# Performance work log

Hardware: AMD Instinct MI355X
Metric: run time of the kernel (lower is better)

Reference implementation:

```python
import jax, jax.numpy as jnp
import numpy as np

B, L, D, W = 4, 256, 256, 8  # batch, seq_len, d_model, context_window
NS_EPS = 1e-7


def setup_inputs() -> dict:
    key = jax.random.key(0)
    ks = jax.random.split(key, 12)
    f = lambda k, s: jax.random.normal(k, s, dtype=jnp.float32)
    sD = 1.0 / np.sqrt(D)
    return {
        "x": f(ks[0], (B, L, D)),
        "k_aligned": jnp.tanh(f(ks[1], (B, L, D))),  # QKProjectionLayer applies tanh upstream
        "v": f(ks[2], (B, L, D)),
        "M_prev": f(ks[3], (B, D, D)) * 0.01,
        "S_prev": jnp.zeros((B, D, D), jnp.float32),
        # polynomial feature coeffs: phi(k) = c1*k + c2*k^2 (degree 2, dim-preserving)
        "poly_coeffs": jnp.stack([jnp.ones((D,), jnp.float32), 0.1 * jnp.ones((D,), jnp.float32)])
        + 0.01 * f(ks[4], (2, D)),
        "alpha_W": f(ks[5], (D, D)) * sD, "alpha_b": jnp.zeros((D,), jnp.float32),
        "eta_W": f(ks[6], (D, D)) * sD, "eta_b": jnp.zeros((D,), jnp.float32),
        "theta_W": f(ks[7], (D, D)) * sD, "theta_b": jnp.zeros((D,), jnp.float32),
        "gamma_W": f(ks[8], (D,)) * sD, "gamma_b": jnp.zeros((1,), jnp.float32),
        "out_W": f(ks[9], (D, D)) * sD, "out_b": jnp.zeros((D,), jnp.float32),
    }


def _newton_schulz_1(S):
    # NS_K with K=1: X <- 1.5*X - 0.5*X X^T X after Frobenius normalization
    norm = jnp.sqrt(jnp.sum(S * S, axis=(-2, -1), keepdims=True)) + NS_EPS
    X = S / norm
    return 1.5 * X - 0.5 * jnp.einsum('bij,bkj,bkl->bil', X, X, X)


def reference(x, k_aligned, v, M_prev, S_prev, poly_coeffs,
              alpha_W, alpha_b, eta_W, eta_b, theta_W, theta_b,
              gamma_W, gamma_b, out_W, out_b):
    Bn, Ln, Dn = x.shape
    # polynomial feature layer (dim-preserving, degree 2)
    k_phi = poly_coeffs[0] * k_aligned + poly_coeffs[1] * k_aligned ** 2  # [B,L,D]
    # per-token gates (precomputed, pure linear+sigmoid)
    alpha = jax.nn.sigmoid(x @ alpha_W.T + alpha_b)          # [B,L,D]
    eta = jax.nn.sigmoid(x @ eta_W.T + eta_b) * 0.1          # [B,L,D]
    theta = jax.nn.sigmoid(x @ theta_W.T + theta_b)          # [B,L,D]
    gamma = jax.nn.sigmoid(jnp.einsum('bld,d->bl', x, gamma_W) + gamma_b[0])  # [B,L]
    c_arr = jnp.minimum(jnp.arange(Ln) + 1, W).astype(x.dtype)  # actual window length per step

    to_t = lambda a: jnp.moveaxis(a, 1, 0)  # [B,L,...] -> [L,B,...]
    xs = (to_t(k_phi), to_t(v), to_t(gamma), to_t(alpha), to_t(eta), to_t(theta), c_arr)

    buf_k = jnp.zeros((Bn, W, Dn), x.dtype)  # sliding window of phi(k); zero pads contribute 0
    buf_v = jnp.zeros((Bn, W, Dn), x.dtype)
    buf_g = jnp.zeros((Bn, W), x.dtype)

    def step(carry, xt):
        M, S, bk, bv, bg = carry
        k_t, v_t, g_t, a_t, e_t, th_t, c_t = xt
        bk = jnp.concatenate([bk[:, 1:], k_t[:, None]], axis=1)
        bv = jnp.concatenate([bv[:, 1:], v_t[:, None]], axis=1)
        bg = jnp.concatenate([bg[:, 1:], g_t[:, None]], axis=1)
        # Omega gradient: sum_i gamma_i * (M phi(k_i) - v_i) outer phi(k_i) / c
        pred = jnp.einsum('bde,bwe->bwd', M, bk)
        err = pred - bv
        grad = jnp.einsum('bw,bwd,bwe->bde', bg, err, bk) / c_t
        S = th_t[..., None] * S + grad
        S_ortho = _newton_schulz_1(S)
        M = a_t[..., None] * M - e_t[..., None] * S_ortho
        y = jnp.einsum('bde,be->bd', M, k_t)
        return (M, S, bk, bv, bg), y

    (M, S, _, _, _), ys = jax.lax.scan(step, (M_prev, S_prev, buf_k, buf_v, buf_g), xs)
    output = jnp.moveaxis(ys, 0, 1) @ out_W.T + out_b  # out_proj per token
    return (output, M, S)
```

## Files before the change

kernel.cpp:

```cpp
#include <hip/hip_runtime.h>

#define Bn 4
#define Ln 256
#define Dn 256
#define Wn 8
#define NBLK 64
#define BLD (Bn*Ln*Dn)
#define BDD (Bn*Dn*Dn)

typedef float  floatx4 __attribute__((ext_vector_type(4)));
typedef short  short8  __attribute__((ext_vector_type(8)));

__device__ __forceinline__ float ldc(const float* p) {
    return __hip_atomic_load(p, __ATOMIC_RELAXED, __HIP_MEMORY_SCOPE_AGENT);
}
__device__ __forceinline__ void stc(float* p, float v) {
    __hip_atomic_store(p, v, __ATOMIC_RELAXED, __HIP_MEMORY_SCOPE_AGENT);
}
__device__ __forceinline__ void stc4(float* p, floatx4 v) {
    asm volatile("global_store_dwordx4 %0, %1, off sc0 sc1" :: "v"(p), "v"(v) : "memory");
}
__device__ __forceinline__ void ldc4x4(floatx4& a0, floatx4& a1, floatx4& a2, floatx4& a3,
    const float* p0, const float* p1, const float* p2, const float* p3)
{
    asm volatile(
        "global_load_dwordx4 %0, %4, off sc0 sc1\n\t"
        "global_load_dwordx4 %1, %5, off sc0 sc1\n\t"
        "global_load_dwordx4 %2, %6, off sc0 sc1\n\t"
        "global_load_dwordx4 %3, %7, off sc0 sc1\n\t"
        "s_waitcnt vmcnt(0)"
        : "=&v"(a0), "=&v"(a1), "=&v"(a2), "=&v"(a3)
        : "v"(p0), "v"(p1), "v"(p2), "v"(p3)
        : "memory");
}
__device__ __forceinline__ void ldc4x8(
    floatx4& a0, floatx4& a1, floatx4& a2, floatx4& a3,
    floatx4& b0, floatx4& b1, floatx4& b2, floatx4& b3,
    const float* p0, const float* p1, const float* p2, const float* p3,
    const float* q0, const float* q1, const float* q2, const float* q3)
{
    asm volatile(
        "global_load_dwordx4 %0, %8, off sc0 sc1\n\t"
        "global_load_dwordx4 %1, %9, off sc0 sc1\n\t"
        "global_load_dwordx4 %2, %10, off sc0 sc1\n\t"
        "global_load_dwordx4 %3, %11, off sc0 sc1\n\t"
        "global_load_dwordx4 %4, %12, off sc0 sc1\n\t"
        "global_load_dwordx4 %5, %13, off sc0 sc1\n\t"
        "global_load_dwordx4 %6, %14, off sc0 sc1\n\t"
        "global_load_dwordx4 %7, %15, off sc0 sc1\n\t"
        "s_waitcnt vmcnt(0)"
        : "=&v"(a0), "=&v"(a1), "=&v"(a2), "=&v"(a3),
          "=&v"(b0), "=&v"(b1), "=&v"(b2), "=&v"(b3)
        : "v"(p0), "v"(p1), "v"(p2), "v"(p3),
          "v"(q0), "v"(q1), "v"(q2), "v"(q3)
        : "memory");
}

__device__ __forceinline__ unsigned f2bf(float x) {
    unsigned u = __float_as_uint(x);
    return (u + 0x7FFFu + ((u >> 16) & 1u)) >> 16;
}
__device__ __forceinline__ unsigned long long packbf4(floatx4 v) {
    unsigned lo = f2bf(v[0]) | (f2bf(v[1]) << 16);
    unsigned hi = f2bf(v[2]) | (f2bf(v[3]) << 16);
    return (unsigned long long)lo | ((unsigned long long)hi << 32);
}
union BF8 { short8 s8; unsigned long long u[2]; };

__device__ __forceinline__ void grid_sync(unsigned* flags, unsigned k)
{
    asm volatile("s_waitcnt vmcnt(0) lgkmcnt(0)" ::: "memory");
    __syncthreads();
    if (threadIdx.x == 0)
        __hip_atomic_store(&flags[(unsigned)blockIdx.x * 32u], k,
                           __ATOMIC_RELAXED, __HIP_MEMORY_SCOPE_AGENT);
    if (threadIdx.x < NBLK) {
        while (__hip_atomic_load(&flags[(unsigned)threadIdx.x * 32u],
                                 __ATOMIC_RELAXED, __HIP_MEMORY_SCOPE_AGENT) < k)
            __builtin_amdgcn_s_sleep(1);
    }
    __syncthreads();
}

__global__ __launch_bounds__(256) void kphi_gamma_kernel(
    const float* __restrict__ k_al, const float* __restrict__ x,
    const float* __restrict__ poly, const float* __restrict__ gW,
    const float* __restrict__ gb, float* __restrict__ kphi,
    float* __restrict__ gamma)
{
    int wg = blockIdx.x, tid = threadIdx.x;
    int wave = tid >> 6, lane = tid & 63;
    int n = wg * 4 + wave;
    float gacc = 0.f;
#pragma unroll
    for (int c = 0; c < 4; ++c) {
        int e = lane + 64 * c;
        float kv = k_al[n * Dn + e];
        kphi[n * Dn + e] = poly[e] * kv + poly[Dn + e] * kv * kv;
        gacc += x[n * Dn + e] * gW[e];
    }
#pragma unroll
    for (int off = 32; off; off >>= 1) gacc += __shfl_xor(gacc, off);
    if (lane == 0) gamma[n] = 1.f / (1.f + expf(-(gacc + gb[0])));
}

template <int ACT>
__global__ __launch_bounds__(256) void gemm_act_kernel(
    const float* __restrict__ In, const float* __restrict__ Wm,
    const float* __restrict__ bias, float* __restrict__ Out)
{
    __shared__ float ldsX[32 * 64];
    __shared__ float ldsW[64 * 65];
    int n0 = blockIdx.x * 32;
    int m0 = blockIdx.y * 64;
    int tid = threadIdx.x;
    float acc[8] = {0, 0, 0, 0, 0, 0, 0, 0};
    for (int j0 = 0; j0 < 256; j0 += 64) {
#pragma unroll
        for (int q = 0; q < 2; ++q) {
            int fi = tid + 256 * q; int row = fi >> 4; int c4 = (fi & 15) << 2;
            *(float4*)&ldsX[row * 64 + c4] =
                *(const float4*)&In[(n0 + row) * 256 + j0 + c4];
        }
#pragma unroll
        for (int q = 0; q < 4; ++q) {
            int fi = tid + 256 * q; int row = fi >> 4; int c4 = (fi & 15) << 2;
            float4 vv = *(const float4*)&Wm[(m0 + row) * 256 + j0 + c4];
            ldsW[(c4 + 0) * 65 + row] = vv.x;
            ldsW[(c4 + 1) * 65 + row] = vv.y;
            ldsW[(c4 + 2) * 65 + row] = vv.z;
            ldsW[(c4 + 3) * 65 + row] = vv.w;
        }
        __syncthreads();
        int m = tid & 63, ng = tid >> 6;
        for (int j = 0; j < 64; ++j) {
            float wv = ldsW[j * 65 + m];
#pragma unroll
            for (int r = 0; r < 8; ++r) acc[r] += ldsX[(ng * 8 + r) * 64 + j] * wv;
        }
        __syncthreads();
    }
    int m = tid & 63, ng = tid >> 6;
    float bv = bias[m0 + m];
#pragma unroll
    for (int r = 0; r < 8; ++r) {
        float vv = acc[r] + bv;
        if (ACT == 1) vv = 1.f / (1.f + expf(-vv));
        if (ACT == 2) vv = 0.1f / (1.f + expf(-vv));
        Out[(n0 + ng * 8 + r) * 256 + m0 + m] = vv;
    }
}

__global__ __launch_bounds__(64) void kgram_kernel(
    const float* __restrict__ kphi, float* __restrict__ Kall)
{
    int t = blockIdx.x, b = blockIdx.y, tid = threadIdx.x;
    int wa = tid >> 3, wb = tid & 7;
    int ta = t - 7 + wa, tb = t - 7 + wb;
    float g = 0.f;
    if (ta >= 0 && tb >= 0) {
        const float* pa = &kphi[(b * Ln + ta) * Dn];
        const float* pb = &kphi[(b * Ln + tb) * Dn];
        for (int j = 0; j < Dn; j += 4) {
            floatx4 x1 = *(const floatx4*)&pa[j];
            floatx4 x2 = *(const floatx4*)&pb[j];
            g += x1[0]*x2[0] + x1[1]*x2[1] + x1[2]*x2[2] + x1[3]*x2[3];
        }
    }
    Kall[(b * Ln + t) * 64 + tid] = g;
}

__global__ __launch_bounds__(256) void prologue_kernel(
    float* __restrict__ ys, float* __restrict__ errp,
    float* __restrict__ normbuf, unsigned* __restrict__ flags)
{
    int gidx = blockIdx.x * 256 + threadIdx.x;
    float4 z = {0.f, 0.f, 0.f, 0.f};
    ((float4*)ys)[gidx] = z;
    if (gidx < 4096) ((float4*)errp)[gidx] = z;
    if (gidx < 256)  ((float4*)normbuf)[gidx] = z;
    if (gidx < 512)  {
        uint4 zu = {0u,0u,0u,0u};
        ((uint4*)flags)[gidx] = zu;
    }
}

#define OFF_T      0
#define OFF_ST     16640
#define OFF_UV     25088
#define OFF_AV     27136
#define OFF_CV     29184
#define OFF_TH     31232
#define OFF_KT     31488
#define OFF_KW2    31744
#define OFF_KWA    33792
#define OFF_KL     35872
#define OFF_SRED   35936

__global__ void __launch_bounds__(256, 1) scan_kernel(
    const float* __restrict__ kphi, const float* __restrict__ vin,
    const float* __restrict__ gammaB, const float* __restrict__ alphaB,
    const float* __restrict__ etaB, const float* __restrict__ thetaB,
    const float* __restrict__ Kall,
    const float* __restrict__ Mprev, const float* __restrict__ Sprev,
    unsigned short* __restrict__ STg,
    float* __restrict__ u_buf, float* __restrict__ a_buf,
    float* __restrict__ errp_g, float* __restrict__ normbuf,
    float* __restrict__ ysg, unsigned* __restrict__ flags,
    float* __restrict__ outM, float* __restrict__ outS)
{
    __shared__ float smem[36000];
    float* T_lds = smem + OFF_T;
    float* uv    = smem + OFF_UV;
    float* av    = smem + OFF_AV;
    float* cv    = smem + OFF_CV;
    float* thv   = smem + OFF_TH;
    float* kT    = smem + OFF_KT;
    float* kW2   = smem + OFF_KW2;
    float* kWA   = smem + OFF_KWA;
    float* Kl    = smem + OFF_KL;
    float* sred  = smem + OFF_SRED;

    const int wg = blockIdx.x, tid = threadIdx.x;
    const int b   = wg >> 4;
    const int rem = wg & 15;
    const int i0 = (rem >> 2) * 64, l0 = (rem & 3) * 64;
    const int d0 = rem << 4;
    const int wid = tid >> 6, lane = tid & 63;
    const int lme = lane & 15, hi = lane >> 4;
    const int ibr = i0 + wid * 16 + (hi << 2);
    const int r  = tid >> 4, m = tid & 15;
    const int e0 = m * 16;
    unsigned kbar = 0;

    floatx4 S_reg[4];
    float   M_reg[16];

    {
#pragma unroll
        for (int cq = 0; cq < 4; ++cq)
            S_reg[cq] = *(const floatx4*)&Sprev[(size_t)(b*256 + d0 + r)*256 + e0 + cq*4];
#pragma unroll
        for (int lt = 0; lt < 4; ++lt)
#pragma unroll
            for (int g = 0; g < 4; ++g)
                M_reg[lt*4+g] = Mprev[(size_t)(b*256 + ibr + g)*256 + l0 + lt*16 + lme];

        for (int g4 = 0; g4 < 4; ++g4) {
            floatx4 acc[4];
#pragma unroll
            for (int lt = 0; lt < 4; ++lt) acc[lt] = (floatx4){0.f,0.f,0.f,0.f};
#pragma unroll
            for (int kc = 0; kc < 8; ++kc) {
                int kb2 = kc*32 + hi*8;
                floatx4 a0 = *(const floatx4*)&Sprev[(size_t)(b*256 + i0 + wid*16 + lme)*256 + kb2];
                floatx4 a1 = *(const floatx4*)&Sprev[(size_t)(b*256 + i0 + wid*16 + lme)*256 + kb2 + 4];
                BF8 ua; ua.u[0] = packbf4(a0); ua.u[1] = packbf4(a1);
#pragma unroll
                for (int lt = 0; lt < 4; ++lt) {
                    int brow = g4*64 + lt*16 + lme;
                    floatx4 b0 = *(const floatx4*)&Sprev[(size_t)(b*256 + brow)*256 + kb2];
                    floatx4 b1 = *(const floatx4*)&Sprev[(size_t)(b*256 + brow)*256 + kb2 + 4];
                    BF8 ub; ub.u[0] = packbf4(b0); ub.u[1] = packbf4(b1);
                    acc[lt] = __builtin_amdgcn_mfma_f32_16x16x32_bf16(ua.s8, ub.s8, acc[lt], 0,0,0);
                }
            }
#pragma unroll
            for (int lt = 0; lt < 4; ++lt)
#pragma unroll
                for (int g = 0; g < 4; ++g)
                    T_lds[(wid*16 + (hi<<2) + g)*260 + g4*64 + lt*16 + lme] = acc[lt][g];
        }

#pragma unroll
        for (int q = 0; q < 2; ++q) {
            int w = q*4 + (tid >> 6);
            int c4 = (tid & 63) << 2;
            floatx4 kv = {0.f,0.f,0.f,0.f};
            if (w == 7) kv = *(const floatx4*)&kphi[(size_t)(b*Ln)*Dn + c4];
            *(floatx4*)&kW2[w*256 + c4] = kv;
        }
        __syncthreads();
#pragma unroll
        for (int w = 0; w < 8; ++w) {
            float pd[4] = {0.f,0.f,0.f,0.f};
#pragma unroll
            for (int lt = 0; lt < 4; ++lt) {
                float kv2 = kW2[w*256 + l0 + lt*16 + lme];
#pragma unroll
                for (int g = 0; g < 4; ++g) pd[g] += M_reg[lt*4+g] * kv2;
            }
#pragma unroll
            for (int g = 0; g < 4; ++g) {
                pd[g] += __shfl_xor(pd[g], 1); pd[g] += __shfl_xor(pd[g], 2);
                pd[g] += __shfl_xor(pd[g], 4); pd[g] += __shfl_xor(pd[g], 8);
            }
            if (lme == 0)
#pragma unroll
                for (int g = 0; g < 4; ++g)
                    atomicAdd(&errp_g[(size_t)(0*4 + b)*2048 + w*256 + ibr + g], pd[g]);
        }
    }
    grid_sync(flags, ++kbar);

    for (int t = 0; t < Ln; ++t) {
        const int cwin = (t + 1 < Wn) ? (t + 1) : Wn;
        const float invc = 1.f / (float)cwin;

        {
#pragma unroll
            for (int q = 0; q < 2; ++q) {
                int w = q*4 + (tid >> 6);
                int c4 = (tid & 63) << 2;
                int tk = t - 7 + w;
                floatx4 kv = {0.f,0.f,0.f,0.f};
                if (tk >= 0) kv = *(const floatx4*)&kphi[(size_t)(b*Ln + tk)*Dn + c4];
                *(floatx4*)&kWA[w*260 + c4] = kv;
            }
            __syncthreads();

            {
                float qw[8] = {0,0,0,0,0,0,0,0};
#pragma unroll
                for (int cq = 0; cq < 4; ++cq) {
                    floatx4 sv = S_reg[cq];
#pragma unroll
                    for (int w = 0; w < 8; ++w) {
                        floatx4 kv = *(const floatx4*)&kWA[w*260 + e0 + cq*4];
                        qw[w] += sv[0]*kv[0] + sv[1]*kv[1] + sv[2]*kv[2] + sv[3]*kv[3];
                    }
                }
#pragma unroll
                for (int w = 0; w < 8; ++w) {
                    qw[w] += __shfl_xor(qw[w], 1); qw[w] += __shfl_xor(qw[w], 2);
                    qw[w] += __shfl_xor(qw[w], 4); qw[w] += __shfl_xor(qw[w], 8);
                }
                if (m < 8) {
                    float th = thetaB[(size_t)(b*Ln + t)*Dn + d0 + r];
                    stc(&a_buf[(size_t)(b*8 + m)*256 + d0 + r], th * qw[m]);
                }
            }
            if (tid < 128) {
                int w = tid >> 4, rr = tid & 15;
                float* epp = &errp_g[(size_t)((t&1)*4 + b)*2048 + w*256 + d0 + rr];
                float ep = ldc(epp);
                stc(epp, 0.f);
                int tok = t - 7 + w;
                float uu = 0.f;
                if (tok >= 0)
                    uu = gammaB[b*Ln + tok] * invc *
                         (ep - vin[(size_t)(b*Ln + tok)*Dn + d0 + rr]);
                uv[w*16 + rr] = uu;
                stc(&u_buf[(size_t)(b*8 + w)*256 + d0 + rr], uu);
            }
            __syncthreads();

            {
                float th = thetaB[(size_t)(b*Ln + t)*Dn + d0 + r];
                float uu[8];
#pragma unroll
                for (int w = 0; w < 8; ++w) uu[w] = uv[w*16 + r];
                float sumsq = 0.f;
#pragma unroll
                for (int cq = 0; cq < 4; ++cq) {
                    floatx4 sv = th * S_reg[cq];
#pragma unroll
                    for (int w = 0; w < 8; ++w) {
                        floatx4 kv = *(const floatx4*)&kWA[w*260 + e0 + cq*4];
                        sv += uu[w] * kv;
                    }
                    S_reg[cq] = sv;
                    sumsq += sv[0]*sv[0] + sv[1]*sv[1] + sv[2]*sv[2] + sv[3]*sv[3];
                }
#pragma unroll
                for (int off = 32; off; off >>= 1) sumsq += __shfl_xor(sumsq, off);
                if ((tid & 63) == 0) atomicAdd(&normbuf[t*4 + b], sumsq);
            }

            {
                float* Sl = smem + OFF_ST;
#pragma unroll
                for (int cq = 0; cq < 4; ++cq)
                    *(floatx4*)&Sl[r*260 + e0 + cq*4] = S_reg[cq];
                __syncthreads();
                int l = tid;
                unsigned dw[8];
#pragma unroll
                for (int j = 0; j < 8; ++j)
                    dw[j] = f2bf(Sl[(2*j)*260 + l]) | (f2bf(Sl[(2*j+1)*260 + l]) << 16);
                floatx4 p0 = { __uint_as_float(dw[0]), __uint_as_float(dw[1]),
                               __uint_as_float(dw[2]), __uint_as_float(dw[3]) };
                floatx4 p1 = { __uint_as_float(dw[4]), __uint_as_float(dw[5]),
                               __uint_as_float(dw[6]), __uint_as_float(dw[7]) };
                char* dstp = (char*)STg + ((size_t)(b*256 + l)*256 + d0)*2;
                stc4((float*)dstp, p0);
                stc4((float*)(dstp + 16), p1);
            }
            if (t == Ln - 1) {
#pragma unroll
                for (int cq = 0; cq < 4; ++cq)
                    *(floatx4*)&outS[(size_t)(b*256 + d0 + r)*256 + e0 + cq*4] = S_reg[cq];
            }
        }
        grid_sync(flags, ++kbar);

        {
            {
                int lq = tid >> 2, kq = (tid & 3) * 64;
                const char* src = (const char*)STg + ((size_t)(b*256 + l0 + lq)*256 + kq)*2;
                floatx4 r0,r1,r2,r3,r4,r5,r6,r7;
                ldc4x8(r0,r1,r2,r3,r4,r5,r6,r7,
                       (const float*)(src+0),  (const float*)(src+16),
                       (const float*)(src+32), (const float*)(src+48),
                       (const float*)(src+64), (const float*)(src+80),
                       (const float*)(src+96), (const float*)(src+112));
                char* dst = (char*)(smem + OFF_ST) + (lq*264 + kq)*2;
                *(floatx4*)(dst+0)  = r0; *(floatx4*)(dst+16) = r1;
                *(floatx4*)(dst+32) = r2; *(floatx4*)(dst+48) = r3;
                *(floatx4*)(dst+64) = r4; *(floatx4*)(dst+80) = r5;
                *(floatx4*)(dst+96) = r6; *(floatx4*)(dst+112)= r7;

                floatx4 u0,u1,a0,a1;
                ldc4x4(u0,u1,a0,a1,
                       &u_buf[(size_t)b*2048 + tid*8], &u_buf[(size_t)b*2048 + tid*8 + 4],
                       &a_buf[(size_t)b*2048 + tid*8], &a_buf[(size_t)b*2048 + tid*8 + 4]);
                *(floatx4*)&uv[tid*8]     = u0; *(floatx4*)&uv[tid*8 + 4] = u1;
                *(floatx4*)&av[tid*8]     = a0; *(floatx4*)&av[tid*8 + 4] = a1;

                if (tid < 64) {
                    *(floatx4*)&thv[tid*4] = *(const floatx4*)&thetaB[(size_t)(b*Ln + t)*Dn + tid*4];
                    *(floatx4*)&kT[tid*4]  = *(const floatx4*)&kphi[(size_t)(b*Ln + t)*Dn + tid*4];
                }
                if (tid < 16)
                    *(floatx4*)&Kl[tid*4] = *(const floatx4*)&Kall[(size_t)(b*Ln + t)*64 + tid*4];
                if (t < Ln - 1) {
#pragma unroll
                    for (int q = 0; q < 2; ++q) {
                        int w = q*4 + (tid >> 6);
                        int c4 = (tid & 63) << 2;
                        int tk = t + 1 - 7 + w;
                        floatx4 kv = {0.f,0.f,0.f,0.f};
                        if (tk >= 0) kv = *(const floatx4*)&kphi[(size_t)(b*Ln + tk)*Dn + c4];
                        *(floatx4*)&kW2[w*256 + c4] = kv;
                    }
                }
                if (tid == 0) sred[0] = ldc(&normbuf[t*4 + b]);
            }
            __syncthreads();

#pragma unroll
            for (int q = 0; q < 8; ++q) {
                int idx = q*256 + tid;
                int w = idx >> 8, e = idx & 255;
                float s = av[idx];
#pragma unroll
                for (int w2 = 0; w2 < 8; ++w2)
                    s += 0.5f * Kl[w*8 + w2] * uv[w2*256 + e];
                cv[idx] = s;
            }
            __syncthreads();

            {
                int ig = tid >> 4;
                int iloc0 = ig * 4;
                int kg = (tid & 15) * 16;
                floatx4 thi = *(const floatx4*)&thv[i0 + iloc0];
                floatx4 thk[4], Trow[4][4];
#pragma unroll
                for (int j = 0; j < 4; ++j) thk[j] = *(const floatx4*)&thv[kg + 4*j];
#pragma unroll
                for (int ii = 0; ii < 4; ++ii)
#pragma unroll
                    for (int j = 0; j < 4; ++j) {
                        Trow[ii][j] = *(const floatx4*)&T_lds[(iloc0+ii)*260 + kg + 4*j];
                        Trow[ii][j] = (thi[ii] * thk[j]) * Trow[ii][j];
                    }
#pragma unroll
                for (int w = 0; w < 8; ++w) {
                    floatx4 ui4 = *(const floatx4*)&uv[w*256 + i0 + iloc0];
                    floatx4 ci4 = *(const floatx4*)&cv[w*256 + i0 + iloc0];
                    floatx4 uk[4], ck[4];
#pragma unroll
                    for (int j = 0; j < 4; ++j) {
                        uk[j] = *(const floatx4*)&uv[w*256 + kg + 4*j];
                        ck[j] = *(const floatx4*)&cv[w*256 + kg + 4*j];
                    }
#pragma unroll
                    for (int ii = 0; ii < 4; ++ii)
#pragma unroll
                        for (int j = 0; j < 4; ++j)
                            Trow[ii][j] += ui4[ii]*ck[j] + ci4[ii]*uk[j];
                }
#pragma unroll
                for (int ii = 0; ii < 4; ++ii)
#pragma unroll
                    for (int j = 0; j < 4; ++j)
                        *(floatx4*)&T_lds[(iloc0+ii)*260 + kg + 4*j] = Trow[ii][j];
            }
            __syncthreads();

            floatx4 acc[4];
#pragma unroll
            for (int lt = 0; lt < 4; ++lt) acc[lt] = (floatx4){0.f,0.f,0.f,0.f};
#pragma unroll
            for (int kc = 0; kc < 8; ++kc) {
                int kb2 = kc*32 + hi*8;
                floatx4 a0 = *(const floatx4*)&T_lds[(wid*16 + lme)*260 + kb2];
                floatx4 a1 = *(const floatx4*)&T_lds[(wid*16 + lme)*260 + kb2 + 4];
                BF8 ua; ua.u[0] = packbf4(a0); ua.u[1] = packbf4(a1);
#pragma unroll
                for (int lt = 0; lt < 4; ++lt) {
                    short8 bf = *(const short8*)((const char*)(smem + OFF_ST)
                                  + ((lt*16 + lme)*264 + kb2)*2);
                    acc[lt] = __builtin_amdgcn_mfma_f32_16x16x32_bf16(ua.s8, bf, acc[lt], 0,0,0);
                }
            }

            {
                float nsq = sred[0];
                float nrm = sqrtf(nsq) + 1e-7f;
                float inv_n = 1.f / nrm;
                float w1 = 1.5f * inv_n;
                float w3 = 0.5f * inv_n * inv_n * inv_n;
                float alv[4], etv[4], kvr[4];
#pragma unroll
                for (int g = 0; g < 4; ++g) {
                    alv[g] = alphaB[(size_t)(b*Ln + t)*Dn + ibr + g];
                    etv[g] = etaB[(size_t)(b*Ln + t)*Dn + ibr + g];
                }
#pragma unroll
                for (int lt = 0; lt < 4; ++lt) kvr[lt] = kT[l0 + lt*16 + lme];
                float py[4] = {0.f,0.f,0.f,0.f};
#pragma unroll
                for (int lt = 0; lt < 4; ++lt)
#pragma unroll
                    for (int g = 0; g < 4; ++g) {
                        int l_loc = lt*16 + lme;
                        unsigned short sb = *(const unsigned short*)
                            ((const char*)(smem + OFF_ST) + (l_loc*264 + ibr + g)*2);
                        float s_il = __uint_as_float(((unsigned)sb) << 16);
                        float ns = w1 * s_il - w3 * acc[lt][g];
                        float mn = alv[g] * M_reg[lt*4+g] - etv[g] * ns;
                        M_reg[lt*4+g] = mn;
                        py[g] += mn * kvr[lt];
                        if (t == Ln - 1)
                            outM[(size_t)(b*256 + ibr + g)*256 + l0 + l_loc] = mn;
                    }
#pragma unroll
                for (int g = 0; g < 4; ++g) {
                    py[g] += __shfl_xor(py[g], 1); py[g] += __shfl_xor(py[g], 2);
                    py[g] += __shfl_xor(py[g], 4); py[g] += __shfl_xor(py[g], 8);
                    if (lme == 0) atomicAdd(&ysg[(size_t)(b*Ln + t)*Dn + ibr + g], py[g]);
                }
            }

            if (t < Ln - 1) {
#pragma unroll
                for (int w = 0; w < 8; ++w) {
                    float pd[4] = {0.f,0.f,0.f,0.f};
#pragma unroll
                    for (int lt = 0; lt < 4; ++lt) {
                        float kv2 = kW2[w*256 + l0 + lt*16 + lme];
#pragma unroll
                        for (int g = 0; g < 4; ++g) pd[g] += M_reg[lt*4+g] * kv2;
                    }
#pragma unroll
                    for (int g = 0; g < 4; ++g) {
                        pd[g] += __shfl_xor(pd[g], 1); pd[g] += __shfl_xor(pd[g], 2);
                        pd[g] += __shfl_xor(pd[g], 4); pd[g] += __shfl_xor(pd[g], 8);
                    }
                    if (lme == 0)
#pragma unroll
                        for (int g = 0; g < 4; ++g)
                            atomicAdd(&errp_g[(size_t)(((t+1)&1)*4 + b)*2048 + w*256 + ibr + g], pd[g]);
                }
            }
        }
        grid_sync(flags, ++kbar);
    }
}

extern "C" void kernel_launch(void* const* d_in, const int* in_sizes, int n_in,
                              void* d_out, int out_size, void* d_ws, size_t ws_size,
                              hipStream_t stream)
{
    const float* x       = (const float*)d_in[0];
    const float* k_al    = (const float*)d_in[1];
    const float* v       = (const float*)d_in[2];
    const float* M_prev  = (const float*)d_in[3];
    const float* S_prev  = (const float*)d_in[4];
    const float* poly    = (const float*)d_in[5];
    const float* alpha_W = (const float*)d_in[6];
    const float* alpha_b = (const float*)d_in[7];
    const float* eta_W   = (const float*)d_in[8];
    const float* eta_b   = (const float*)d_in[9];
    const float* theta_W = (const float*)d_in[10];
    const float* theta_b = (const float*)d_in[11];
    const float* gamma_W = (const float*)d_in[12];
    const float* gamma_b = (const float*)d_in[13];
    const float* out_W   = (const float*)d_in[14];
    const float* out_b   = (const float*)d_in[15];

    float* ws = (float*)d_ws;
    float* kphi    = ws;
    float* alphaB  = kphi   + BLD;
    float* etaB    = alphaB + BLD;
    float* thetaB  = etaB   + BLD;
    float* gammaB  = thetaB + BLD;
    float* Kall    = gammaB + Bn*Ln;
    float* STg_f   = Kall   + Bn*Ln*64;
    float* u_bufp  = STg_f  + 131072;
    float* a_bufp  = u_bufp + Bn*Wn*Dn;
    float* errp    = a_bufp + Bn*Wn*Dn;
    float* normbuf = errp   + 16384;
    float* ysws    = normbuf + Ln*Bn;
    unsigned* flags = (unsigned*)(ysws + BLD);

    float* out_y = (float*)d_out;
    float* outM  = out_y + BLD;
    float* outS  = outM + BDD;

    hipLaunchKernelGGL(kphi_gamma_kernel, dim3(256), dim3(256), 0, stream,
                       k_al, x, poly, gamma_W, gamma_b, kphi, gammaB);
    hipLaunchKernelGGL((gemm_act_kernel<1>), dim3(32, 4), dim3(256), 0, stream,
                       x, alpha_W, alpha_b, alphaB);
    hipLaunchKernelGGL((gemm_act_kernel<2>), dim3(32, 4), dim3(256), 0, stream,
                       x, eta_W, eta_b, etaB);
    hipLaunchKernelGGL((gemm_act_kernel<1>), dim3(32, 4), dim3(256), 0, stream,
                       x, theta_W, theta_b, thetaB);
    hipLaunchKernelGGL(kgram_kernel, dim3(Ln, Bn), dim3(64), 0, stream,
                       kphi, Kall);
    hipLaunchKernelGGL(prologue_kernel, dim3(256), dim3(256), 0, stream,
                       ysws, errp, normbuf, flags);

    hipLaunchKernelGGL(scan_kernel, dim3(NBLK), dim3(256), 0, stream,
                       kphi, v, gammaB, alphaB, etaB, thetaB, Kall,
                       M_prev, S_prev, (unsigned short*)STg_f,
                       u_bufp, a_bufp, errp, normbuf, ysws, flags,
                       outM, outS);

    hipLaunchKernelGGL((gemm_act_kernel<0>), dim3(32, 4), dim3(256), 0, stream,
                       ysws, out_W, out_b, out_y);
}
```

Measured before the change: 6.245 ms.

## Use per-batch barriers, atomic-free partial buffers, register-resident T, swizzled LDS

The grid barrier now spans only the 16 workgroups that share a batch instead of all 64. Atomic adds into the error, norm and output buffers are replaced with per-slice plain stores, summed by readers or by a new ysum reduction kernel. The T matrix now lives in registers, the S-transpose LDS tile is XOR-swizzled, and the u/a/norm loads are merged into one batched load to cut waits. The cost is more workspace, an extra kernel launch, and higher register pressure from T_reg.

Result: faster. 5.753 ms (-7.9%).

```diff
diff --git a/kernel.cpp b/kernel.cpp
--- a/kernel.cpp
+++ b/kernel.cpp
@@ -20,39 +20,48 @@
 __device__ __forceinline__ void stc4(float* p, floatx4 v) {
     asm volatile("global_store_dwordx4 %0, %1, off sc0 sc1" :: "v"(p), "v"(v) : "memory");
 }
-__device__ __forceinline__ void ldc4x4(floatx4& a0, floatx4& a1, floatx4& a2, floatx4& a3,
+__device__ __forceinline__ void ldc1x4(float& a, float& b, float& c, float& d,
     const float* p0, const float* p1, const float* p2, const float* p3)
 {
     asm volatile(
-        "global_load_dwordx4 %0, %4, off sc0 sc1\n\t"
-        "global_load_dwordx4 %1, %5, off sc0 sc1\n\t"
-        "global_load_dwordx4 %2, %6, off sc0 sc1\n\t"
-        "global_load_dwordx4 %3, %7, off sc0 sc1\n\t"
+        "global_load_dword %0, %4, off sc0 sc1\n\t"
+        "global_load_dword %1, %5, off sc0 sc1\n\t"
+        "global_load_dword %2, %6, off sc0 sc1\n\t"
+        "global_load_dword %3, %7, off sc0 sc1\n\t"
         "s_waitcnt vmcnt(0)"
-        : "=&v"(a0), "=&v"(a1), "=&v"(a2), "=&v"(a3)
+        : "=&v"(a), "=&v"(b), "=&v"(c), "=&v"(d)
         : "v"(p0), "v"(p1), "v"(p2), "v"(p3)
         : "memory");
 }
-__device__ __forceinline__ void ldc4x8(
-    floatx4& a0, floatx4& a1, floatx4& a2, floatx4& a3,
-    floatx4& b0, floatx4& b1, floatx4& b2, floatx4& b3,
+__device__ __forceinline__ void ldc4x12s(
+    floatx4& r0, floatx4& r1, floatx4& r2, floatx4& r3,
+    floatx4& r4, floatx4& r5, floatx4& r6, floatx4& r7,
+    floatx4& r8, floatx4& r9, floatx4& r10, floatx4& r11, float& sc,
     const float* p0, const float* p1, const float* p2, const float* p3,
-    const float* q0, const float* q1, const float* q2, const float* q3)
+    const float* p4, const float* p5, const float* p6, const float* p7,
+    const float* p8, const float* p9, const float* p10, const float* p11,
+    const float* ps)
 {
     asm volatile(
-        "global_load_dwordx4 %0, %8, off sc0 sc1\n\t"
-        "global_load_dwordx4 %1, %9, off sc0 sc1\n\t"
-        "global_load_dwordx4 %2, %10, off sc0 sc1\n\t"
-        "global_load_dwordx4 %3, %11, off sc0 sc1\n\t"
-        "global_load_dwordx4 %4, %12, off sc0 sc1\n\t"
-        "global_load_dwordx4 %5, %13, off sc0 sc1\n\t"
-        "global_load_dwordx4 %6, %14, off sc0 sc1\n\t"
-        "global_load_dwordx4 %7, %15, off sc0 sc1\n\t"
+        "global_load_dwordx4 %0, %13, off sc0 sc1\n\t"
+        "global_load_dwordx4 %1, %14, off sc0 sc1\n\t"
+        "global_load_dwordx4 %2, %15, off sc0 sc1\n\t"
+        "global_load_dwordx4 %3, %16, off sc0 sc1\n\t"
+        "global_load_dwordx4 %4, %17, off sc0 sc1\n\t"
+        "global_load_dwordx4 %5, %18, off sc0 sc1\n\t"
+        "global_load_dwordx4 %6, %19, off sc0 sc1\n\t"
+        "global_load_dwordx4 %7, %20, off sc0 sc1\n\t"
+        "global_load_dwordx4 %8, %21, off sc0 sc1\n\t"
+        "global_load_dwordx4 %9, %22, off sc0 sc1\n\t"
+        "global_load_dwordx4 %10, %23, off sc0 sc1\n\t"
+        "global_load_dwordx4 %11, %24, off sc0 sc1\n\t"
+        "global_load_dword %12, %25, off sc0 sc1\n\t"
         "s_waitcnt vmcnt(0)"
-        : "=&v"(a0), "=&v"(a1), "=&v"(a2), "=&v"(a3),
-          "=&v"(b0), "=&v"(b1), "=&v"(b2), "=&v"(b3)
-        : "v"(p0), "v"(p1), "v"(p2), "v"(p3),
-          "v"(q0), "v"(q1), "v"(q2), "v"(q3)
+        : "=&v"(r0), "=&v"(r1), "=&v"(r2), "=&v"(r3),
+          "=&v"(r4), "=&v"(r5), "=&v"(r6), "=&v"(r7),
+          "=&v"(r8), "=&v"(r9), "=&v"(r10), "=&v"(r11), "=&v"(sc)
+        : "v"(p0), "v"(p1), "v"(p2), "v"(p3), "v"(p4), "v"(p5),
+          "v"(p6), "v"(p7), "v"(p8), "v"(p9), "v"(p10), "v"(p11), "v"(ps)
         : "memory");
 }
 
@@ -67,15 +76,15 @@
 }
 union BF8 { short8 s8; unsigned long long u[2]; };
 
-__device__ __forceinline__ void grid_sync(unsigned* flags, unsigned k)
+__device__ __forceinline__ void grid_sync_b(unsigned* bflags, int rem, unsigned k)
 {
     asm volatile("s_waitcnt vmcnt(0) lgkmcnt(0)" ::: "memory");
     __syncthreads();
     if (threadIdx.x == 0)
-        __hip_atomic_store(&flags[(unsigned)blockIdx.x * 32u], k,
+        __hip_atomic_store(&bflags[rem * 32], k,
                            __ATOMIC_RELAXED, __HIP_MEMORY_SCOPE_AGENT);
-    if (threadIdx.x < NBLK) {
-        while (__hip_atomic_load(&flags[(unsigned)threadIdx.x * 32u],
+    if (threadIdx.x < 16) {
+        while (__hip_atomic_load(&bflags[threadIdx.x * 32],
                                  __ATOMIC_RELAXED, __HIP_MEMORY_SCOPE_AGENT) < k)
             __builtin_amdgcn_s_sleep(1);
     }
@@ -170,32 +179,43 @@
     Kall[(b * Ln + t) * 64 + tid] = g;
 }
 
-__global__ __launch_bounds__(256) void prologue_kernel(
-    float* __restrict__ ys, float* __restrict__ errp,
-    float* __restrict__ normbuf, unsigned* __restrict__ flags)
+__global__ __launch_bounds__(256) void prologue_kernel(unsigned* __restrict__ flags)
 {
     int gidx = blockIdx.x * 256 + threadIdx.x;
-    float4 z = {0.f, 0.f, 0.f, 0.f};
-    ((float4*)ys)[gidx] = z;
-    if (gidx < 4096) ((float4*)errp)[gidx] = z;
-    if (gidx < 256)  ((float4*)normbuf)[gidx] = z;
-    if (gidx < 512)  {
-        uint4 zu = {0u,0u,0u,0u};
+    if (gidx < 512) {
+        uint4 zu = {0u, 0u, 0u, 0u};
         ((uint4*)flags)[gidx] = zu;
     }
 }
 
-#define OFF_T      0
-#define OFF_ST     16640
-#define OFF_UV     25088
-#define OFF_AV     27136
-#define OFF_CV     29184
-#define OFF_TH     31232
-#define OFF_KT     31488
-#define OFF_KW2    31744
-#define OFF_KWA    33792
-#define OFF_KL     35872
-#define OFF_SRED   35936
+__global__ __launch_bounds__(256) void ysum_kernel(float* __restrict__ ysp)
+{
+    int gidx = blockIdx.x * 256 + threadIdx.x;
+    float4 a = ((float4*)ysp)[gidx];
+    float4 b = ((float4*)ysp)[65536 + gidx];
+    float4 c = ((float4*)ysp)[131072 + gidx];
+    float4 d = ((float4*)ysp)[196608 + gidx];
+    a.x += b.x + c.x + d.x;
+    a.y += b.y + c.y + d.y;
+    a.z += b.z + c.z + d.z;
+    a.w += b.w + c.w + d.w;
+    ((float4*)ysp)[gidx] = a;
+}
+
+#define OFF_ST    0
+#define OFF_UV    8448
+#define OFF_AV    10496
+#define OFF_CV    12544
+#define OFF_TH    14592
+#define OFF_KT    14848
+#define OFF_KL    15104
+#define OFF_NRM   15168
+#define OFF_WSUM  15184
+#define OFF_US    15200
+#define OFF_KWA   15328
+#define OFF_KW2   17408
+#define OFF_SL    19456
+#define SMEM_FLOATS 23616
 
 __global__ void __launch_bounds__(256, 1) scan_kernel(
     const float* __restrict__ kphi, const float* __restrict__ vin,
@@ -205,47 +225,53 @@
     const float* __restrict__ Mprev, const float* __restrict__ Sprev,
     unsigned short* __restrict__ STg,
     float* __restrict__ u_buf, float* __restrict__ a_buf,
-    float* __restrict__ errp_g, float* __restrict__ normbuf,
-    float* __restrict__ ysg, unsigned* __restrict__ flags,
+    float* __restrict__ errp_g, float* __restrict__ normp,
+    float* __restrict__ ysp, unsigned* __restrict__ flags,
     float* __restrict__ outM, float* __restrict__ outS)
 {
-    __shared__ float smem[36000];
-    float* T_lds = smem + OFF_T;
-    float* uv    = smem + OFF_UV;
-    float* av    = smem + OFF_AV;
-    float* cv    = smem + OFF_CV;
-    float* thv   = smem + OFF_TH;
-    float* kT    = smem + OFF_KT;
-    float* kW2   = smem + OFF_KW2;
-    float* kWA   = smem + OFF_KWA;
-    float* Kl    = smem + OFF_KL;
-    float* sred  = smem + OFF_SRED;
+    __shared__ float smem[SMEM_FLOATS];
+    char*  STb  = (char*)(smem + OFF_ST);
+    float* uvp  = smem + OFF_UV;
+    float* avp  = smem + OFF_AV;
+    float* cvp  = smem + OFF_CV;
+    float* thv  = smem + OFF_TH;
+    float* kT   = smem + OFF_KT;
+    float* Kl   = smem + OFF_KL;
+    float* nrml = smem + OFF_NRM;
+    float* wsum = smem + OFF_WSUM;
+    float* usl  = smem + OFF_US;
+    float* kWA  = smem + OFF_KWA;
+    float* kW2  = smem + OFF_KW2;
+    float* Sl   = smem + OFF_SL;
 
     const int wg = blockIdx.x, tid = threadIdx.x;
     const int b   = wg >> 4;
     const int rem = wg & 15;
+    const int s   = rem & 3;
     const int i0 = (rem >> 2) * 64, l0 = (rem & 3) * 64;
     const int d0 = rem << 4;
     const int wid = tid >> 6, lane = tid & 63;
     const int lme = lane & 15, hi = lane >> 4;
     const int ibr = i0 + wid * 16 + (hi << 2);
     const int r  = tid >> 4, m = tid & 15;
-    const int e0 = m * 16;
+    unsigned* bflags = flags + b * 512;
     unsigned kbar = 0;
 
     floatx4 S_reg[4];
     float   M_reg[16];
+    floatx4 T_reg[16];
 
     {
 #pragma unroll
         for (int cq = 0; cq < 4; ++cq)
-            S_reg[cq] = *(const floatx4*)&Sprev[(size_t)(b*256 + d0 + r)*256 + e0 + cq*4];
+            S_reg[cq] = *(const floatx4*)&Sprev[(size_t)(b*256 + d0 + r)*256 + m*4 + 64*cq];
 #pragma unroll
         for (int lt = 0; lt < 4; ++lt)
 #pragma unroll
             for (int g = 0; g < 4; ++g)
                 M_reg[lt*4+g] = Mprev[(size_t)(b*256 + ibr + g)*256 + l0 + lt*16 + lme];
 
+        float* scratch = smem;
         for (int g4 = 0; g4 < 4; ++g4) {
             floatx4 acc[4];
 #pragma unroll
@@ -269,9 +295,14 @@
             for (int lt = 0; lt < 4; ++lt)
 #pragma unroll
                 for (int g = 0; g < 4; ++g)
-                    T_lds[(wid*16 + (hi<<2) + g)*260 + g4*64 + lt*16 + lme] = acc[lt][g];
-        }
-
+                    scratch[(wid*16 + (hi<<2) + g)*260 + g4*64 + lt*16 + lme] = acc[lt][g];
+        }
+        __syncthreads();
+#pragma unroll
+        for (int kc = 0; kc < 8; ++kc) {
+            T_reg[kc*2+0] = *(floatx4*)&scratch[(wid*16 + lme)*260 + kc*32 + hi*8];
+            T_reg[kc*2+1] = *(floatx4*)&scratch[(wid*16 + lme)*260 + kc*32 + hi*8 + 4];
+        }
 #pragma unroll
         for (int q = 0; q < 2; ++q) {
             int w = q*4 + (tid >> 6);
@@ -298,24 +329,45 @@
             if (lme == 0)
 #pragma unroll
                 for (int g = 0; g < 4; ++g)
-                    atomicAdd(&errp_g[(size_t)(0*4 + b)*2048 + w*256 + ibr + g], pd[g]);
-        }
-    }
-    grid_sync(flags, ++kbar);
+                    stc(&errp_g[(size_t)((s*2 + 0)*4 + b)*2048 + w*256 + ibr + g], pd[g]);
+        }
+    }
+    grid_sync_b(bflags, rem, ++kbar);
 
     for (int t = 0; t < Ln; ++t) {
         const int cwin = (t + 1 < Wn) ? (t + 1) : Wn;
         const float invc = 1.f / (float)cwin;
 
         {
-#pragma unroll
-            for (int q = 0; q < 2; ++q) {
-                int w = q*4 + (tid >> 6);
-                int c4 = (tid & 63) << 2;
+            float e0_ = 0.f, e1_ = 0.f, e2_ = 0.f, e3_ = 0.f;
+            int w_a = 0, rr_a = 0;
+            const int p = t & 1;
+            if (tid < 128) {
+                w_a = tid >> 4; rr_a = tid & 15;
+                ldc1x4(e0_, e1_, e2_, e3_,
+                    &errp_g[(size_t)((0*2 + p)*4 + b)*2048 + w_a*256 + d0 + rr_a],
+                    &errp_g[(size_t)((1*2 + p)*4 + b)*2048 + w_a*256 + d0 + rr_a],
+                    &errp_g[(size_t)((2*2 + p)*4 + b)*2048 + w_a*256 + d0 + rr_a],
+                    &errp_g[(size_t)((3*2 + p)*4 + b)*2048 + w_a*256 + d0 + rr_a]);
+                float ep = e0_ + e1_ + e2_ + e3_;
+                int tok = t - 7 + w_a;
+                float uu = 0.f;
+                if (tok >= 0)
+                    uu = gammaB[b*Ln + tok] * invc *
+                         (ep - vin[(size_t)(b*Ln + tok)*Dn + d0 + rr_a]);
+                usl[w_a*16 + rr_a] = uu;
+                stc(&u_buf[(size_t)(b*8 + w_a)*256 + d0 + rr_a], uu);
+            } else {
+                int idx = tid - 128;
+                int w = idx >> 4, seg = idx & 15;
                 int tk = t - 7 + w;
-                floatx4 kv = {0.f,0.f,0.f,0.f};
-                if (tk >= 0) kv = *(const floatx4*)&kphi[(size_t)(b*Ln + tk)*Dn + c4];
-                *(floatx4*)&kWA[w*260 + c4] = kv;
+#pragma unroll
+                for (int q = 0; q < 4; ++q) {
+                    floatx4 kv = {0.f,0.f,0.f,0.f};
+                    if (tk >= 0)
+                        kv = *(const floatx4*)&kphi[(size_t)(b*Ln + tk)*Dn + seg*16 + q*4];
+                    *(floatx4*)&kWA[w*260 + seg*16 + q*4] = kv;
+                }
             }
             __syncthreads();
 
@@ -326,7 +378,7 @@
                     floatx4 sv = S_reg[cq];
 #pragma unroll
                     for (int w = 0; w < 8; ++w) {
-                        floatx4 kv = *(const floatx4*)&kWA[w*260 + e0 + cq*4];
+                        floatx4 kv = *(const floatx4*)&kWA[w*260 + m*4 + 64*cq];
                         qw[w] += sv[0]*kv[0] + sv[1]*kv[1] + sv[2]*kv[2] + sv[3]*kv[3];
                     }
                 }
@@ -340,33 +392,18 @@
                     stc(&a_buf[(size_t)(b*8 + m)*256 + d0 + r], th * qw[m]);
                 }
             }
-            if (tid < 128) {
-                int w = tid >> 4, rr = tid & 15;
-                float* epp = &errp_g[(size_t)((t&1)*4 + b)*2048 + w*256 + d0 + rr];
-                float ep = ldc(epp);
-                stc(epp, 0.f);
-                int tok = t - 7 + w;
-                float uu = 0.f;
-                if (tok >= 0)
-                    uu = gammaB[b*Ln + tok] * invc *
-                         (ep - vin[(size_t)(b*Ln + tok)*Dn + d0 + rr]);
-                uv[w*16 + rr] = uu;
-                stc(&u_buf[(size_t)(b*8 + w)*256 + d0 + rr], uu);
-            }
-            __syncthreads();
-
             {
                 float th = thetaB[(size_t)(b*Ln + t)*Dn + d0 + r];
                 float uu[8];
 #pragma unroll
-                for (int w = 0; w < 8; ++w) uu[w] = uv[w*16 + r];
+                for (int w = 0; w < 8; ++w) uu[w] = usl[w*16 + r];
                 float sumsq = 0.f;
 #pragma unroll
                 for (int cq = 0; cq < 4; ++cq) {
                     floatx4 sv = th * S_reg[cq];
 #pragma unroll
                     for (int w = 0; w < 8; ++w) {
-                        floatx4 kv = *(const floatx4*)&kWA[w*260 + e0 + cq*4];
+                        floatx4 kv = *(const floatx4*)&kWA[w*260 + m*4 + 64*cq];
                         sv += uu[w] * kv;
                     }
                     S_reg[cq] = sv;
@@ -374,14 +411,12 @@
                 }
 #pragma unroll
                 for (int off = 32; off; off >>= 1) sumsq += __shfl_xor(sumsq, off);
-                if ((tid & 63) == 0) atomicAdd(&normbuf[t*4 + b], sumsq);
-            }
-
+                if (lane == 0) wsum[wid] = sumsq;
+            }
             {
-                float* Sl = smem + OFF_ST;
 #pragma unroll
                 for (int cq = 0; cq < 4; ++cq)
-                    *(floatx4*)&Sl[r*260 + e0 + cq*4] = S_reg[cq];
+                    *(floatx4*)&Sl[r*260 + m*4 + 64*cq] = S_reg[cq];
                 __syncthreads();
                 int l = tid;
                 unsigned dw[8];
@@ -395,38 +430,44 @@
                 char* dstp = (char*)STg + ((size_t)(b*256 + l)*256 + d0)*2;
                 stc4((float*)dstp, p0);
                 stc4((float*)(dstp + 16), p1);
+                if (tid == 0)
+                    stc(&normp[b*16 + rem], wsum[0] + wsum[1] + wsum[2] + wsum[3]);
             }
             if (t == Ln - 1) {
 #pragma unroll
                 for (int cq = 0; cq < 4; ++cq)
-                    *(floatx4*)&outS[(size_t)(b*256 + d0 + r)*256 + e0 + cq*4] = S_reg[cq];
-            }
-        }
-        grid_sync(flags, ++kbar);
+                    *(floatx4*)&outS[(size_t)(b*256 + d0 + r)*256 + m*4 + 64*cq] = S_reg[cq];
+            }
+        }
+        grid_sync_b(bflags, rem, ++kbar);
 
         {
             {
                 int lq = tid >> 2, kq = (tid & 3) * 64;
                 const char* src = (const char*)STg + ((size_t)(b*256 + l0 + lq)*256 + kq)*2;
-                floatx4 r0,r1,r2,r3,r4,r5,r6,r7;
-                ldc4x8(r0,r1,r2,r3,r4,r5,r6,r7,
-                       (const float*)(src+0),  (const float*)(src+16),
-                       (const float*)(src+32), (const float*)(src+48),
-                       (const float*)(src+64), (const float*)(src+80),
-                       (const float*)(src+96), (const float*)(src+112));
-                char* dst = (char*)(smem + OFF_ST) + (lq*264 + kq)*2;
-                *(floatx4*)(dst+0)  = r0; *(floatx4*)(dst+16) = r1;
-                *(floatx4*)(dst+32) = r2; *(floatx4*)(dst+48) = r3;
-                *(floatx4*)(dst+64) = r4; *(floatx4*)(dst+80) = r5;
-                *(floatx4*)(dst+96) = r6; *(floatx4*)(dst+112)= r7;
-
-                floatx4 u0,u1,a0,a1;
-                ldc4x4(u0,u1,a0,a1,
-                       &u_buf[(size_t)b*2048 + tid*8], &u_buf[(size_t)b*2048 + tid*8 + 4],
-                       &a_buf[(size_t)b*2048 + tid*8], &a_buf[(size_t)b*2048 + tid*8 + 4]);
-                *(floatx4*)&uv[tid*8]     = u0; *(floatx4*)&uv[tid*8 + 4] = u1;
-                *(floatx4*)&av[tid*8]     = a0; *(floatx4*)&av[tid*8 + 4] = a1;
-
+                const float* pu = &u_buf[(size_t)b*2048 + tid*8];
+                const float* pa = &a_buf[(size_t)b*2048 + tid*8];
+                const float* pn = (tid < 16) ? &normp[b*16 + tid] : pu;
+                floatx4 r0,r1,r2,r3,r4,r5,r6,r7,u0,u1,a0,a1; float nsc;
+                ldc4x12s(r0,r1,r2,r3,r4,r5,r6,r7,u0,u1,a0,a1,nsc,
+                    (const float*)(src+0),  (const float*)(src+16),
+                    (const float*)(src+32), (const float*)(src+48),
+                    (const float*)(src+64), (const float*)(src+80),
+                    (const float*)(src+96), (const float*)(src+112),
+                    pu, pu+4, pa, pa+4, pn);
+                size_t rb0 = (size_t)lq*528 + (size_t)kq*2;
+                unsigned swz = (unsigned)((lq & 8) << 1);
+                *(floatx4*)(STb + ((rb0 +   0) ^ swz)) = r0;
+                *(floatx4*)(STb + ((rb0 +  16) ^ swz)) = r1;
+                *(floatx4*)(STb + ((rb0 +  32) ^ swz)) = r2;
+                *(floatx4*)(STb + ((rb0 +  48) ^ swz)) = r3;
+                *(floatx4*)(STb + ((rb0 +  64) ^ swz)) = r4;
+                *(floatx4*)(STb + ((rb0 +  80) ^ swz)) = r5;
+                *(floatx4*)(STb + ((rb0 +  96) ^ swz)) = r6;
+                *(floatx4*)(STb + ((rb0 + 112) ^ swz)) = r7;
+                *(floatx4*)&uvp[tid*8]     = u0; *(floatx4*)&uvp[tid*8 + 4] = u1;
+                *(floatx4*)&avp[tid*8]     = a0; *(floatx4*)&avp[tid*8 + 4] = a1;
+                if (tid < 16) nrml[tid] = nsc;
                 if (tid < 64) {
                     *(floatx4*)&thv[tid*4] = *(const floatx4*)&thetaB[(size_t)(b*Ln + t)*Dn + tid*4];
                     *(floatx4*)&kT[tid*4]  = *(const floatx4*)&kphi[(size_t)(b*Ln + t)*Dn + tid*4];
@@ -444,7 +485,6 @@
                         *(floatx4*)&kW2[w*256 + c4] = kv;
                     }
                 }
-                if (tid == 0) sred[0] = ldc(&normbuf[t*4 + b]);
             }
             __syncthreads();
 
@@ -452,72 +492,61 @@
             for (int q = 0; q < 8; ++q) {
                 int idx = q*256 + tid;
                 int w = idx >> 8, e = idx & 255;
-                float s = av[idx];
+                float sv = avp[idx];
 #pragma unroll
                 for (int w2 = 0; w2 < 8; ++w2)
-                    s += 0.5f * Kl[w*8 + w2] * uv[w2*256 + e];
-                cv[idx] = s;
+                    sv += 0.5f * Kl[w*8 + w2] * uvp[w2*256 + e];
+                cvp[idx] = sv;
             }
             __syncthreads();
 
             {
-                int ig = tid >> 4;
-                int iloc0 = ig * 4;
-                int kg = (tid & 15) * 16;
-                floatx4 thi = *(const floatx4*)&thv[i0 + iloc0];
-                floatx4 thk[4], Trow[4][4];
-#pragma unroll
-                for (int j = 0; j < 4; ++j) thk[j] = *(const floatx4*)&thv[kg + 4*j];
-#pragma unroll
-                for (int ii = 0; ii < 4; ++ii)
-#pragma unroll
-                    for (int j = 0; j < 4; ++j) {
-                        Trow[ii][j] = *(const floatx4*)&T_lds[(iloc0+ii)*260 + kg + 4*j];
-                        Trow[ii][j] = (thi[ii] * thk[j]) * Trow[ii][j];
+                int i = i0 + wid*16 + lme;
+                float thi = thv[i];
+                float ui8[8], ci8[8];
+#pragma unroll
+                for (int w = 0; w < 8; ++w) { ui8[w] = uvp[w*256 + i]; ci8[w] = cvp[w*256 + i]; }
+#pragma unroll
+                for (int kc = 0; kc < 8; ++kc) {
+                    int k0 = kc*32 + hi*8;
+                    floatx4 th0 = *(const floatx4*)&thv[k0];
+                    floatx4 th1 = *(const floatx4*)&thv[k0 + 4];
+                    floatx4 t0 = (thi * th0) * T_reg[kc*2+0];
+                    floatx4 t1 = (thi * th1) * T_reg[kc*2+1];
+#pragma unroll
+                    for (int w = 0; w < 8; ++w) {
+                        floatx4 uk0 = *(const floatx4*)&uvp[w*256 + k0];
+                        floatx4 uk1 = *(const floatx4*)&uvp[w*256 + k0 + 4];
+                        floatx4 ck0 = *(const floatx4*)&cvp[w*256 + k0];
+                        floatx4 ck1 = *(const floatx4*)&cvp[w*256 + k0 + 4];
+                        t0 += ui8[w]*ck0 + ci8[w]*uk0;
+                        t1 += ui8[w]*ck1 + ci8[w]*uk1;
                     }
-#pragma unroll
-                for (int w = 0; w < 8; ++w) {
-                    floatx4 ui4 = *(const floatx4*)&uv[w*256 + i0 + iloc0];
-                    floatx4 ci4 = *(const floatx4*)&cv[w*256 + i0 + iloc0];
-                    floatx4 uk[4], ck[4];
-#pragma unroll
-                    for (int j = 0; j < 4; ++j) {
-                        uk[j] = *(const floatx4*)&uv[w*256 + kg + 4*j];
-                        ck[j] = *(const floatx4*)&cv[w*256 + kg + 4*j];
-                    }
-#pragma unroll
-                    for (int ii = 0; ii < 4; ++ii)
-#pragma unroll
-                        for (int j = 0; j < 4; ++j)
-                            Trow[ii][j] += ui4[ii]*ck[j] + ci4[ii]*uk[j];
-                }
-#pragma unroll
-                for (int ii = 0; ii < 4; ++ii)
-#pragma unroll
-                    for (int j = 0; j < 4; ++j)
-                        *(floatx4*)&T_lds[(iloc0+ii)*260 + kg + 4*j] = Trow[ii][j];
-            }
-            __syncthreads();
+                    T_reg[kc*2+0] = t0;
+                    T_reg[kc*2+1] = t1;
+                }
+            }
 
             floatx4 acc[4];
 #pragma unroll
             for (int lt = 0; lt < 4; ++lt) acc[lt] = (floatx4){0.f,0.f,0.f,0.f};
 #pragma unroll
             for (int kc = 0; kc < 8; ++kc) {
-                int kb2 = kc*32 + hi*8;
-                floatx4 a0 = *(const floatx4*)&T_lds[(wid*16 + lme)*260 + kb2];
-                floatx4 a1 = *(const floatx4*)&T_lds[(wid*16 + lme)*260 + kb2 + 4];
-                BF8 ua; ua.u[0] = packbf4(a0); ua.u[1] = packbf4(a1);
+                BF8 ua; ua.u[0] = packbf4(T_reg[kc*2]); ua.u[1] = packbf4(T_reg[kc*2+1]);
+                int kbyte = kc*64 + hi*16;
 #pragma unroll
                 for (int lt = 0; lt < 4; ++lt) {
-                    short8 bf = *(const short8*)((const char*)(smem + OFF_ST)
-                                  + ((lt*16 + lme)*264 + kb2)*2);
+                    int row = lt*16 + lme;
+                    short8 bf = *(const short8*)(STb +
+                        (((size_t)row*528 + kbyte) ^ (unsigned)((row & 8) << 1)));
                     acc[lt] = __builtin_amdgcn_mfma_f32_16x16x32_bf16(ua.s8, bf, acc[lt], 0,0,0);
                 }
             }
 
             {
-                float nsq = sred[0];
+                float nsq = 0.f;
+#pragma unroll
+                for (int q = 0; q < 16; ++q) nsq += nrml[q];
                 float nrm = sqrtf(nsq) + 1e-7f;
                 float inv_n = 1.f / nrm;
                 float w1 = 1.5f * inv_n;
@@ -536,8 +565,8 @@
 #pragma unroll
                     for (int g = 0; g < 4; ++g) {
                         int l_loc = lt*16 + lme;
-                        unsigned short sb = *(const unsigned short*)
-                            ((const char*)(smem + OFF_ST) + (l_loc*264 + ibr + g)*2);
+                        unsigned short sb = *(const unsigned short*)(STb +
+                            (((size_t)l_loc*528 + (size_t)(ibr + g)*2) ^ (unsigned)((l_loc & 8) << 1)));
                         float s_il = __uint_as_float(((unsigned)sb) << 16);
                         float ns = w1 * s_il - w3 * acc[lt][g];
                         float mn = alv[g] * M_reg[lt*4+g] - etv[g] * ns;
@@ -550,11 +579,13 @@
                 for (int g = 0; g < 4; ++g) {
                     py[g] += __shfl_xor(py[g], 1); py[g] += __shfl_xor(py[g], 2);
                     py[g] += __shfl_xor(py[g], 4); py[g] += __shfl_xor(py[g], 8);
-                    if (lme == 0) atomicAdd(&ysg[(size_t)(b*Ln + t)*Dn + ibr + g], py[g]);
+                    if (lme == 0)
+                        stc(&ysp[(size_t)s*BLD + (size_t)(b*Ln + t)*Dn + ibr + g], py[g]);
                 }
             }
 
             if (t < Ln - 1) {
+                const int p2 = (t + 1) & 1;
 #pragma unroll
                 for (int w = 0; w < 8; ++w) {
                     float pd[4] = {0.f,0.f,0.f,0.f};
@@ -572,11 +603,11 @@
                     if (lme == 0)
 #pragma unroll
                         for (int g = 0; g < 4; ++g)
-                            atomicAdd(&errp_g[(size_t)(((t+1)&1)*4 + b)*2048 + w*256 + ibr + g], pd[g]);
-                }
-            }
-        }
-        grid_sync(flags, ++kbar);
+                            stc(&errp_g[(size_t)((s*2 + p2)*4 + b)*2048 + w*256 + ibr + g], pd[g]);
+                }
+            }
+        }
+        grid_sync_b(bflags, rem, ++kbar);
     }
 }
 
@@ -612,9 +643,9 @@
     float* u_bufp  = STg_f  + 131072;
     float* a_bufp  = u_bufp + Bn*Wn*Dn;
     float* errp    = a_bufp + Bn*Wn*Dn;
-    float* normbuf = errp   + 16384;
-    float* ysws    = normbuf + Ln*Bn;
-    unsigned* flags = (unsigned*)(ysws + BLD);
+    float* normp   = errp   + 65536;
+    float* ysp     = normp  + 64;
+    unsigned* flags = (unsigned*)(ysp + 4*BLD);
 
     float* out_y = (float*)d_out;
     float* outM  = out_y + BLD;
@@ -630,15 +661,15 @@
                        x, theta_W, theta_b, thetaB);
     hipLaunchKernelGGL(kgram_kernel, dim3(Ln, Bn), dim3(64), 0, stream,
                        kphi, Kall);
-    hipLaunchKernelGGL(prologue_kernel, dim3(256), dim3(256), 0, stream,
-                       ysws, errp, normbuf, flags);
+    hipLaunchKernelGGL(prologue_kernel, dim3(2), dim3(256), 0, stream, flags);
 
     hipLaunchKernelGGL(scan_kernel, dim3(NBLK), dim3(256), 0, stream,
                        kphi, v, gammaB, alphaB, etaB, thetaB, Kall,
                        M_prev, S_prev, (unsigned short*)STg_f,
-                       u_bufp, a_bufp, errp, normbuf, ysws, flags,
+                       u_bufp, a_bufp, errp, normp, ysp, flags,
                        outM, outS);
 
+    hipLaunchKernelGGL(ysum_kernel, dim3(256), dim3(256), 0, stream, ysp);
     hipLaunchKernelGGL((gemm_act_kernel<0>), dim3(32, 4), dim3(256), 0, stream,
-                       ysws, out_W, out_b, out_y);
-}
+                       ysp, out_W, out_b, out_y);
+}
```
